# Kernel tuning notes

Measured on AMD Instinct MI355X. Metric: run time of the kernel, lower is better.

## Reference

```python
import jax, jax.numpy as jnp
import numpy as np

N = 8192
C_IN = 128
C_OUT = 128


def setup_inputs() -> dict:
    key = jax.random.key(0)
    k1, k2, k3, k4 = jax.random.split(key, 4)
    x = jax.random.normal(k1, (N, C_IN), dtype=jnp.float32)
    adj = jax.random.uniform(k2, (N, N), dtype=jnp.float32)
    mask = jax.random.uniform(k3, (N, N), dtype=jnp.float32)
    # nn.Linear(c_in, c_out, bias=False) weight has shape [c_out, c_in]
    W = jax.random.normal(k4, (C_OUT, C_IN), dtype=jnp.float32) * (1.0 / np.sqrt(C_IN))
    return {"x": x, "adj": adj, "mask": mask, "W": W}


def reference(x, adj, mask, W):
    n = adj.shape[0]
    # adj = adj * mask + I  (mask application plus self-loops)
    adj_eff = adj * mask + jnp.eye(n, dtype=adj.dtype)
    # h = x @ W^T  (Linear, no bias), then aggregate: out = adj_eff @ h
    h = jnp.einsum("nc,oc->no", x, W)  # [N, c_out]
    return jnp.matmul(adj_eff, h)       # [N, c_out]
```

## Files before the change

### kernel.cpp

```cpp
#include <hip/hip_runtime.h>
#include <hip/hip_bf16.h>
#include <stdint.h>

#define NROW 8192
#define CD 128
#define SPLITK 8
#define KCHUNK (NROW / SPLITK)

typedef __bf16 bf16_t;
typedef __bf16 bf16x8 __attribute__((ext_vector_type(8)));
typedef float f32x4 __attribute__((ext_vector_type(4)));

__device__ __forceinline__ f32x4 mfma16(bf16x8 a, bf16x8 b, f32x4 c) {
    return __builtin_amdgcn_mfma_f32_16x16x32_bf16(a, b, c, 0, 0, 0);
}

__device__ __forceinline__ bf16x8 load_cvt_bf16(const float* __restrict__ p) {
    float4 a0 = *(const float4*)p;
    float4 a1 = *(const float4*)(p + 4);
    bf16x8 r;
    r[0] = (bf16_t)a0.x; r[1] = (bf16_t)a0.y; r[2] = (bf16_t)a0.z; r[3] = (bf16_t)a0.w;
    r[4] = (bf16_t)a1.x; r[5] = (bf16_t)a1.y; r[6] = (bf16_t)a1.z; r[7] = (bf16_t)a1.w;
    return r;
}

__device__ __forceinline__ bf16x8 load_mul_bf16(const float* __restrict__ pa,
                                                const float* __restrict__ pm) {
    float4 a0 = *(const float4*)pa;
    float4 a1 = *(const float4*)(pa + 4);
    float4 b0 = *(const float4*)pm;
    float4 b1 = *(const float4*)(pm + 4);
    bf16x8 r;
    r[0] = (bf16_t)(a0.x * b0.x); r[1] = (bf16_t)(a0.y * b0.y);
    r[2] = (bf16_t)(a0.z * b0.z); r[3] = (bf16_t)(a0.w * b0.w);
    r[4] = (bf16_t)(a1.x * b1.x); r[5] = (bf16_t)(a1.y * b1.y);
    r[6] = (bf16_t)(a1.z * b1.z); r[7] = (bf16_t)(a1.w * b1.w);
    return r;
}

__global__ void h_kernel(const float* __restrict__ x, const float* __restrict__ W,
                         bf16_t* __restrict__ hT, float* __restrict__ out)
{
    const int wave = threadIdx.x >> 6;
    const int lane = threadIdx.x & 63;
    const int m = lane & 15;
    const int q = lane >> 4;
    const int row_base = blockIdx.x * 128 + wave * 32;

    f32x4 acc[2][8] = {};

#pragma unroll
    for (int k0 = 0; k0 < CD; k0 += 32) {
        bf16x8 af[2];
#pragma unroll
        for (int r = 0; r < 2; ++r)
            af[r] = load_cvt_bf16(x + (size_t)(row_base + r * 16 + m) * CD + k0 + q * 8);
        bf16x8 bfr[8];
#pragma unroll
        for (int c = 0; c < 8; ++c)
            bfr[c] = load_cvt_bf16(W + (size_t)(c * 16 + m) * CD + k0 + q * 8);
#pragma unroll
        for (int r = 0; r < 2; ++r)
#pragma unroll
            for (int c = 0; c < 8; ++c)
                acc[r][c] = mfma16(af[r], bfr[c], acc[r][c]);
    }

#pragma unroll
    for (int r = 0; r < 2; ++r)
#pragma unroll
        for (int c = 0; c < 8; ++c) {
            const int col = c * 16 + m;
#pragma unroll
            for (int j = 0; j < 4; ++j) {
                const int row = row_base + r * 16 + q * 4 + j;
                const float v = acc[r][c][j];
                out[(size_t)row * CD + col] = v;
                hT[(size_t)col * NROW + row] = (bf16_t)v;
            }
        }
}

template <bool ATOMIC>
__global__ void gemm_kernel(const float* __restrict__ adj, const float* __restrict__ mask,
                            const bf16_t* __restrict__ hT, float* __restrict__ outp)
{
    const int wave = threadIdx.x >> 6;
    const int lane = threadIdx.x & 63;
    const int m = lane & 15;
    const int q = lane >> 4;
    const int row_base = blockIdx.x * 128 + wave * 32;
    const int s = blockIdx.y;
    const int kbeg = s * KCHUNK;

    f32x4 acc[2][8] = {};

    const float* pa0 = adj  + (size_t)(row_base + m) * NROW + kbeg + q * 8;
    const float* pa1 = adj  + (size_t)(row_base + 16 + m) * NROW + kbeg + q * 8;
    const float* pm0 = mask + (size_t)(row_base + m) * NROW + kbeg + q * 8;
    const float* pm1 = mask + (size_t)(row_base + 16 + m) * NROW + kbeg + q * 8;
    const bf16_t* pb[8];
#pragma unroll
    for (int c = 0; c < 8; ++c)
        pb[c] = hT + (size_t)(c * 16 + m) * NROW + kbeg + q * 8;

    for (int kk = 0; kk < KCHUNK; kk += 32) {
        bf16x8 af[2];
        af[0] = load_mul_bf16(pa0, pm0);
        af[1] = load_mul_bf16(pa1, pm1);
        pa0 += 32; pa1 += 32; pm0 += 32; pm1 += 32;

        bf16x8 bfr[8];
#pragma unroll
        for (int c = 0; c < 8; ++c) {
            bfr[c] = *(const bf16x8*)(pb[c]);
            pb[c] += 32;
        }

#pragma unroll
        for (int r = 0; r < 2; ++r)
#pragma unroll
            for (int c = 0; c < 8; ++c)
                acc[r][c] = mfma16(af[r], bfr[c], acc[r][c]);
    }

    float* obase = ATOMIC ? outp : outp + (size_t)s * ((size_t)NROW * CD);
#pragma unroll
    for (int r = 0; r < 2; ++r)
#pragma unroll
        for (int c = 0; c < 8; ++c) {
            const int col = c * 16 + m;
#pragma unroll
            for (int j = 0; j < 4; ++j) {
                const int row = row_base + r * 16 + q * 4 + j;
                const size_t idx = (size_t)row * CD + col;
                if (ATOMIC)
                    atomicAdd(outp + idx, acc[r][c][j]);
                else
                    obase[idx] = acc[r][c][j];
            }
        }
}

__global__ void reduce_kernel(float* __restrict__ out, const float* __restrict__ part)
{
    const size_t i = ((size_t)blockIdx.x * 256 + threadIdx.x) * 4;
    float4 sum = *(const float4*)(out + i);
#pragma unroll
    for (int sp = 0; sp < SPLITK; ++sp) {
        float4 p = *(const float4*)(part + (size_t)sp * ((size_t)NROW * CD) + i);
        sum.x += p.x; sum.y += p.y; sum.z += p.z; sum.w += p.w;
    }
    *(float4*)(out + i) = sum;
}

extern "C" void kernel_launch(void* const* d_in, const int* in_sizes, int n_in,
                              void* d_out, int out_size, void* d_ws, size_t ws_size,
                              hipStream_t stream)
{
    const float* x    = (const float*)d_in[0];
    const float* adj  = (const float*)d_in[1];
    const float* mask = (const float*)d_in[2];
    const float* W    = (const float*)d_in[3];
    float* out = (float*)d_out;

    bf16_t* hT = (bf16_t*)d_ws;
    const size_t HT_BYTES   = (size_t)CD * NROW * sizeof(bf16_t);
    const size_t PART_BYTES = (size_t)SPLITK * NROW * CD * sizeof(float);

    h_kernel<<<dim3(64), dim3(256), 0, stream>>>(x, W, hT, out);

    if (ws_size >= HT_BYTES + PART_BYTES) {
        float* part = (float*)((char*)d_ws + HT_BYTES);
        gemm_kernel<false><<<dim3(64, SPLITK), dim3(256), 0, stream>>>(adj, mask, hT, part);
        reduce_kernel<<<dim3(1024), dim3(256), 0, stream>>>(out, part);
    } else {
        gemm_kernel<true><<<dim3(64, SPLITK), dim3(256), 0, stream>>>(adj, mask, hT, out);
    }
}
```

Before: 635.2 us.

## Stage adjacency tiles through swizzled LDS with double buffering and async hT loads

The main GEMM now stages the masked adjacency tile (converted to bf16) and the hT tile in double-buffered, XOR-swizzled shared memory. hT is fetched with global_load_lds DMA, and the next tile's global loads overlap the current tile's MFMAs. Global reads become fully coalesced and each B fragment is shared across all four waves instead of re-read per wave. h_kernel and the gemm epilogue now go through LDS so global stores are coalesced, and h_kernel runs on more blocks. The cost is more LDS use and a barrier every iteration, which may reduce occupancy.

```diff
diff --git a/kernel.cpp b/kernel.cpp
--- a/kernel.cpp
+++ b/kernel.cpp
@@ -6,13 +6,22 @@
 #define CD 128
 #define SPLITK 8
 #define KCHUNK (NROW / SPLITK)
+#define BK 64
+#define NITER (KCHUNK / BK)
 
 typedef __bf16 bf16_t;
 typedef __bf16 bf16x8 __attribute__((ext_vector_type(8)));
+typedef __bf16 bf16x4 __attribute__((ext_vector_type(4)));
 typedef float f32x4 __attribute__((ext_vector_type(4)));
 
 __device__ __forceinline__ f32x4 mfma16(bf16x8 a, bf16x8 b, f32x4 c) {
     return __builtin_amdgcn_mfma_f32_16x16x32_bf16(a, b, c, 0, 0, 0);
+}
+
+__device__ __forceinline__ void dma16(const void* g, void* l) {
+    __builtin_amdgcn_global_load_lds(
+        (const __attribute__((address_space(1))) uint32_t*)g,
+        (__attribute__((address_space(3))) uint32_t*)l, 16, 0, 0);
 }
 
 __device__ __forceinline__ bf16x8 load_cvt_bf16(const float* __restrict__ p) {
@@ -24,122 +33,170 @@
     return r;
 }
 
-__device__ __forceinline__ bf16x8 load_mul_bf16(const float* __restrict__ pa,
-                                                const float* __restrict__ pm) {
-    float4 a0 = *(const float4*)pa;
-    float4 a1 = *(const float4*)(pa + 4);
-    float4 b0 = *(const float4*)pm;
-    float4 b1 = *(const float4*)(pm + 4);
-    bf16x8 r;
-    r[0] = (bf16_t)(a0.x * b0.x); r[1] = (bf16_t)(a0.y * b0.y);
-    r[2] = (bf16_t)(a0.z * b0.z); r[3] = (bf16_t)(a0.w * b0.w);
-    r[4] = (bf16_t)(a1.x * b1.x); r[5] = (bf16_t)(a1.y * b1.y);
-    r[6] = (bf16_t)(a1.z * b1.z); r[7] = (bf16_t)(a1.w * b1.w);
-    return r;
-}
-
-__global__ void h_kernel(const float* __restrict__ x, const float* __restrict__ W,
-                         bf16_t* __restrict__ hT, float* __restrict__ out)
-{
-    const int wave = threadIdx.x >> 6;
-    const int lane = threadIdx.x & 63;
+__global__ __launch_bounds__(256)
+void h_kernel(const float* __restrict__ x, const float* __restrict__ W,
+              bf16_t* __restrict__ hT, float* __restrict__ out)
+{
+    __shared__ __align__(16) float h_sl_all[4][16 * 128];
+    const int tid = threadIdx.x;
+    const int w = tid >> 6, lane = tid & 63;
+    const int m = lane & 15, q = lane >> 4;
+    const int rb = blockIdx.x * 64 + w * 16;
+
+    f32x4 acc[8] = {};
+#pragma unroll
+    for (int k0 = 0; k0 < CD; k0 += 32) {
+        bf16x8 af = load_cvt_bf16(x + (size_t)(rb + m) * CD + k0 + q * 8);
+#pragma unroll
+        for (int c = 0; c < 8; ++c) {
+            bf16x8 bv = load_cvt_bf16(W + (size_t)(c * 16 + m) * CD + k0 + q * 8);
+            acc[c] = mfma16(af, bv, acc[c]);
+        }
+    }
+    float* hs = h_sl_all[w];
+#pragma unroll
+    for (int c = 0; c < 8; ++c)
+#pragma unroll
+        for (int j = 0; j < 4; ++j)
+            hs[(q * 4 + j) * 128 + c * 16 + m] = acc[c][j];
+
+    float* dst = out + (size_t)rb * CD;
+#pragma unroll
+    for (int t = 0; t < 8; ++t) {
+        int fi = t * 64 + lane;
+        *(float4*)(dst + fi * 4) = *(const float4*)(hs + fi * 4);
+    }
+#pragma unroll
+    for (int t = 0; t < 4; ++t) {
+        int idx = t * 64 + lane;
+        int c = idx >> 1, nc = idx & 1;
+        bf16x8 v;
+#pragma unroll
+        for (int j = 0; j < 8; ++j)
+            v[j] = (bf16_t)hs[(nc * 8 + j) * 128 + c];
+        *(bf16x8*)(hT + (size_t)c * NROW + rb + nc * 8) = v;
+    }
+}
+
+template <bool ATOMIC>
+__global__ __launch_bounds__(256)
+void gemm_kernel(const float* __restrict__ adj, const float* __restrict__ mask,
+                 const bf16_t* __restrict__ hT, float* __restrict__ outp)
+{
+    __shared__ __align__(16) ushort lds_all[32768];
+    ushort* const Ab0 = lds_all;
+    ushort* const Ab1 = lds_all + 8192;
+    ushort* const Bb0 = lds_all + 16384;
+    ushort* const Bb1 = lds_all + 24576;
+
+    const int tid  = threadIdx.x;
+    const int w    = tid >> 6;
+    const int lane = tid & 63;
     const int m = lane & 15;
     const int q = lane >> 4;
-    const int row_base = blockIdx.x * 128 + wave * 32;
+    const int rowbase = blockIdx.x * 128;
+    const int kbeg = blockIdx.y * KCHUNK;
 
     f32x4 acc[2][8] = {};
-
-#pragma unroll
-    for (int k0 = 0; k0 < CD; k0 += 32) {
-        bf16x8 af[2];
-#pragma unroll
-        for (int r = 0; r < 2; ++r)
-            af[r] = load_cvt_bf16(x + (size_t)(row_base + r * 16 + m) * CD + k0 + q * 8);
-        bf16x8 bfr[8];
+    float4 va[8], vm[8];
+
+    auto loadA = [&](int it) {
+        const int kw = kbeg + it * BK;
+#pragma unroll
+        for (int rr = 0; rr < 8; ++rr) {
+            int idx = rr * 256 + tid;
+            int row = idx >> 4, c4 = idx & 15;
+            va[rr] = *(const float4*)(adj  + (size_t)(rowbase + row) * NROW + kw + c4 * 4);
+            vm[rr] = *(const float4*)(mask + (size_t)(rowbase + row) * NROW + kw + c4 * 4);
+        }
+    };
+    auto dmaB = [&](int it, ushort* Bb) {
+        const int kw = kbeg + it * BK;
+#pragma unroll
+        for (int rr = 0; rr < 4; ++rr) {
+            int P = w * 256 + rr * 64 + lane;
+            int row = P >> 3;
+            int pc = (P & 7) ^ (row & 7);
+            dma16(hT + (size_t)row * NROW + kw + pc * 8, Bb + (size_t)P * 8);
+        }
+    };
+    auto storeA = [&](ushort* Abuf) {
+#pragma unroll
+        for (int rr = 0; rr < 8; ++rr) {
+            int idx = rr * 256 + tid;
+            int row = idx >> 4, c4 = idx & 15;
+            int sw = (c4 >> 1) ^ (row & 7);
+            bf16x4 v;
+            v[0] = (bf16_t)(va[rr].x * vm[rr].x);
+            v[1] = (bf16_t)(va[rr].y * vm[rr].y);
+            v[2] = (bf16_t)(va[rr].z * vm[rr].z);
+            v[3] = (bf16_t)(va[rr].w * vm[rr].w);
+            *(bf16x4*)(Abuf + row * 64 + sw * 8 + (c4 & 1) * 4) = v;
+        }
+    };
+    auto compute = [&](const ushort* Abuf, const ushort* Bbuf) {
+#pragma unroll
+        for (int ss = 0; ss < 2; ++ss) {
+            const int pc = ss * 4 + q;
+            const int sw = pc ^ (m & 7);
+            bf16x8 af[2];
+#pragma unroll
+            for (int r = 0; r < 2; ++r) {
+                int row = w * 32 + r * 16 + m;
+                af[r] = *(const bf16x8*)(Abuf + row * 64 + sw * 8);
+            }
+#pragma unroll
+            for (int c = 0; c < 8; ++c) {
+                int row = c * 16 + m;
+                bf16x8 bv = *(const bf16x8*)(Bbuf + row * 64 + sw * 8);
+#pragma unroll
+                for (int r = 0; r < 2; ++r)
+                    acc[r][c] = mfma16(af[r], bv, acc[r][c]);
+            }
+        }
+    };
+
+    loadA(0);
+    dmaB(0, Bb0);
+    storeA(Ab0);
+
+    for (int it = 0; it < NITER; ++it) {
+        __syncthreads();
+        const bool nx = (it + 1) < NITER;
+        ushort* An = (it & 1) ? Ab0 : Ab1;
+        ushort* Bn = (it & 1) ? Bb0 : Bb1;
+        const ushort* Ac = (it & 1) ? Ab1 : Ab0;
+        const ushort* Bc = (it & 1) ? Bb1 : Bb0;
+        if (nx) { loadA(it + 1); dmaB(it + 1, Bn); }
+        compute(Ac, Bc);
+        if (nx) storeA(An);
+    }
+
+    __syncthreads();
+    float* h_sl = (float*)lds_all + w * 4096;
+#pragma unroll
+    for (int r = 0; r < 2; ++r)
 #pragma unroll
         for (int c = 0; c < 8; ++c)
-            bfr[c] = load_cvt_bf16(W + (size_t)(c * 16 + m) * CD + k0 + q * 8);
-#pragma unroll
-        for (int r = 0; r < 2; ++r)
-#pragma unroll
-            for (int c = 0; c < 8; ++c)
-                acc[r][c] = mfma16(af[r], bfr[c], acc[r][c]);
-    }
-
-#pragma unroll
-    for (int r = 0; r < 2; ++r)
-#pragma unroll
-        for (int c = 0; c < 8; ++c) {
-            const int col = c * 16 + m;
-#pragma unroll
-            for (int j = 0; j < 4; ++j) {
-                const int row = row_base + r * 16 + q * 4 + j;
-                const float v = acc[r][c][j];
-                out[(size_t)row * CD + col] = v;
-                hT[(size_t)col * NROW + row] = (bf16_t)v;
-            }
-        }
-}
-
-template <bool ATOMIC>
-__global__ void gemm_kernel(const float* __restrict__ adj, const float* __restrict__ mask,
-                            const bf16_t* __restrict__ hT, float* __restrict__ outp)
-{
-    const int wave = threadIdx.x >> 6;
-    const int lane = threadIdx.x & 63;
-    const int m = lane & 15;
-    const int q = lane >> 4;
-    const int row_base = blockIdx.x * 128 + wave * 32;
-    const int s = blockIdx.y;
-    const int kbeg = s * KCHUNK;
-
-    f32x4 acc[2][8] = {};
-
-    const float* pa0 = adj  + (size_t)(row_base + m) * NROW + kbeg + q * 8;
-    const float* pa1 = adj  + (size_t)(row_base + 16 + m) * NROW + kbeg + q * 8;
-    const float* pm0 = mask + (size_t)(row_base + m) * NROW + kbeg + q * 8;
-    const float* pm1 = mask + (size_t)(row_base + 16 + m) * NROW + kbeg + q * 8;
-    const bf16_t* pb[8];
-#pragma unroll
-    for (int c = 0; c < 8; ++c)
-        pb[c] = hT + (size_t)(c * 16 + m) * NROW + kbeg + q * 8;
-
-    for (int kk = 0; kk < KCHUNK; kk += 32) {
-        bf16x8 af[2];
-        af[0] = load_mul_bf16(pa0, pm0);
-        af[1] = load_mul_bf16(pa1, pm1);
-        pa0 += 32; pa1 += 32; pm0 += 32; pm1 += 32;
-
-        bf16x8 bfr[8];
-#pragma unroll
-        for (int c = 0; c < 8; ++c) {
-            bfr[c] = *(const bf16x8*)(pb[c]);
-            pb[c] += 32;
-        }
-
-#pragma unroll
-        for (int r = 0; r < 2; ++r)
-#pragma unroll
-            for (int c = 0; c < 8; ++c)
-                acc[r][c] = mfma16(af[r], bfr[c], acc[r][c]);
-    }
-
-    float* obase = ATOMIC ? outp : outp + (size_t)s * ((size_t)NROW * CD);
-#pragma unroll
-    for (int r = 0; r < 2; ++r)
-#pragma unroll
-        for (int c = 0; c < 8; ++c) {
-            const int col = c * 16 + m;
-#pragma unroll
-            for (int j = 0; j < 4; ++j) {
-                const int row = row_base + r * 16 + q * 4 + j;
-                const size_t idx = (size_t)row * CD + col;
-                if (ATOMIC)
-                    atomicAdd(outp + idx, acc[r][c][j]);
-                else
-                    obase[idx] = acc[r][c][j];
-            }
-        }
+#pragma unroll
+            for (int j = 0; j < 4; ++j)
+                h_sl[(r * 16 + q * 4 + j) * 128 + c * 16 + m] = acc[r][c][j];
+
+    if (!ATOMIC) {
+        float* dst = outp + (size_t)blockIdx.y * ((size_t)NROW * CD)
+                   + (size_t)(rowbase + w * 32) * CD;
+#pragma unroll
+        for (int t = 0; t < 16; ++t) {
+            int fi = t * 64 + lane;
+            *(float4*)(dst + fi * 4) = *(const float4*)(h_sl + fi * 4);
+        }
+    } else {
+        float* dst = outp + (size_t)(rowbase + w * 32) * CD;
+        for (int t = 0; t < 64; ++t) {
+            int ei = t * 64 + lane;
+            atomicAdd(dst + ei, h_sl[ei]);
+        }
+    }
 }
 
 __global__ void reduce_kernel(float* __restrict__ out, const float* __restrict__ part)
@@ -168,7 +225,7 @@
     const size_t HT_BYTES   = (size_t)CD * NROW * sizeof(bf16_t);
     const size_t PART_BYTES = (size_t)SPLITK * NROW * CD * sizeof(float);
 
-    h_kernel<<<dim3(64), dim3(256), 0, stream>>>(x, W, hT, out);
+    h_kernel<<<dim3(NROW / 64), dim3(256), 0, stream>>>(x, W, hT, out);
 
     if (ws_size >= HT_BYTES + PART_BYTES) {
         float* part = (float*)((char*)d_ws + HT_BYTES);
```

Result: faster. 578.7 us (-8.9%).
